# Optimization experiments

Hardware: AMD Instinct MI355X
Metric: run time of the kernel (lower is better)

Reference implementation:

```python
import jax, jax.numpy as jnp
import numpy as np

N_NODES = 100000
N_EDGES = 1600000
IN_CH = 64
HID = 64
N_GRAPHS = 64


def _sage_conv(x, src, dst, Wl, bl, Wr, n_nodes):
    # PyG SAGEConv (aggr='mean'): out = lin_l(mean_{j in N(i)} x_j) + lin_r(x_i)
    msg = x[src]                                            # [E, d] gather
    agg = jax.ops.segment_sum(msg, dst, num_segments=n_nodes)
    cnt = jax.ops.segment_sum(jnp.ones((src.shape[0],), x.dtype), dst,
                              num_segments=n_nodes)
    agg = agg / jnp.maximum(cnt, 1.0)[:, None]
    return agg @ Wl + bl + x @ Wr


def setup_inputs() -> dict:
    key = jax.random.key(0)
    ks = jax.random.split(key, 16)
    x = jax.random.normal(ks[0], (N_NODES, IN_CH), jnp.float32)
    edge_index = jax.random.randint(ks[1], (2, N_EDGES), 0, N_NODES, jnp.int64)
    batch = jnp.sort(jax.random.randint(ks[2], (N_NODES,), 0, N_GRAPHS, jnp.int64))

    def glorot(k, fan_in, fan_out):
        s = jnp.sqrt(2.0 / (fan_in + fan_out))
        return jax.random.normal(k, (fan_in, fan_out), jnp.float32) * s

    params = {
        'W1l': glorot(ks[3], IN_CH, HID), 'b1': jnp.zeros((HID,), jnp.float32),
        'W1r': glorot(ks[4], IN_CH, HID),
        'W2l': glorot(ks[5], HID, HID), 'b2': jnp.zeros((HID,), jnp.float32),
        'W2r': glorot(ks[6], HID, HID),
        'W3l': glorot(ks[7], HID, HID), 'b3': jnp.zeros((HID,), jnp.float32),
        'W3r': glorot(ks[8], HID, HID),
        'Wc1': glorot(ks[9], HID, HID // 2), 'bc1': jnp.zeros((HID // 2,), jnp.float32),
        'Wc2': glorot(ks[10], HID // 2, 2), 'bc2': jnp.zeros((2,), jnp.float32),
    }
    return {'x': x, 'edge_index': edge_index, 'batch': batch, **params}


def reference(x, edge_index, batch,
              W1l, b1, W1r, W2l, b2, W2r, W3l, b3, W3r,
              Wc1, bc1, Wc2, bc2):
    src, dst = edge_index[0], edge_index[1]
    n = x.shape[0]
    h = jax.nn.relu(_sage_conv(x, src, dst, W1l, b1, W1r, n))   # dropout = identity (eval)
    h = jax.nn.relu(_sage_conv(h, src, dst, W2l, b2, W2r, n))
    h = jax.nn.relu(_sage_conv(h, src, dst, W3l, b3, W3r, n))
    # global mean pool over graphs
    sums = jax.ops.segment_sum(h, batch, num_segments=N_GRAPHS)
    cnts = jax.ops.segment_sum(jnp.ones((n,), h.dtype), batch, num_segments=N_GRAPHS)
    g = sums / jnp.maximum(cnts, 1.0)[:, None]                  # [G, HID]
    # MLP head (dropout = identity at eval)
    return jax.nn.relu(g @ Wc1 + bc1) @ Wc2 + bc2               # [G, 2]
```

## Files before the change

kernel.cpp:

```cpp
#include <hip/hip_runtime.h>
#include <hip/hip_bf16.h>
#include <hip/hip_fp16.h>

typedef unsigned int u32;
typedef unsigned short u16;
typedef _Float16 f16x8 __attribute__((ext_vector_type(8)));
typedef float f32x4 __attribute__((ext_vector_type(4)));

#define NBLK1 512
#define CVTBLK 256
#define WPREP 6

__device__ __forceinline__ u16 f2h(float f) { return __half_as_ushort(__float2half(f)); }
__device__ __forceinline__ u32 packh2(float a, float b) {
    return (u32)f2h(a) | ((u32)f2h(b) << 16);
}

__device__ __forceinline__ int gidx(const void* p, long long i, int w64) {
    if (w64) return (int)((const long long*)p)[i];
    return ((const int*)p)[i];
}

__device__ __forceinline__ int detect_w64(const int* edge_words, int E, int tid, int* sh) {
    if (tid == 0) *sh = 0;
    __syncthreads();
    const long long totalWords = 2LL * E;
    const long long step = totalWords / 256;
    long long w = ((long long)tid * step) | 1;
    int nz = (w < totalWords) ? edge_words[w] : 0;
    if (nz) atomicOr(sh, 1);
    __syncthreads();
    return (*sh) ? 0 : 1;
}

__global__ void __launch_bounds__(256) fused_hist_cvt(
        const void* __restrict__ edge, int* __restrict__ flag, u32* __restrict__ ticket,
        u32* __restrict__ HG, int E, int n, int nb1,
        const float* __restrict__ X, u16* __restrict__ Xh,
        const float* __restrict__ W1l, const float* __restrict__ W1r,
        const float* __restrict__ W2l, const float* __restrict__ W2r,
        const float* __restrict__ W3l, const float* __restrict__ W3r,
        _Float16* __restrict__ WFrag) {
    const int tid = threadIdx.x;
    if (blockIdx.x < NBLK1) {
        __shared__ u32 h[256];
        __shared__ int shnz;
        h[tid] = 0;
        const int w64 = detect_w64((const int*)edge, E, tid, &shnz);
        if (blockIdx.x == 0 && tid == 0) { flag[0] = w64; ticket[0] = 0; }
        __syncthreads();
        const int chunk = (E + NBLK1 - 1) / NBLK1;
        const int s = blockIdx.x * chunk;
        const int e = min(s + chunk, E);
        for (int i = s + tid; i < e; i += 256) {
            int d = gidx(edge, (long long)E + i, w64);
            if ((unsigned)d >= (unsigned)n) d = 0;
            atomicAdd(&h[d >> 9], 1);
        }
        __syncthreads();
        for (int b = tid; b < nb1; b += 256) HG[b * NBLK1 + blockIdx.x] = h[b];
        return;
    }
    if (blockIdx.x >= NBLK1 + CVTBLK) {
        const int b = blockIdx.x - NBLK1 - CVTBLK;
        const float* Ws[WPREP] = {W1l, W1r, W2l, W2r, W3l, W3r};
        const float* src = Ws[b];
        _Float16* dst = WFrag + b * 4096;
        for (int idx = tid; idx < 4096; idx += 256) {
            const int k = idx >> 6, c = idx & 63;
            const int d = ((((k >> 5) * 4 + ((k >> 3) & 3)) * 4 + (c >> 4)) * 16 + (c & 15)) * 8
                          + (k & 7);
            dst[d] = (_Float16)src[idx];
        }
        return;
    }
    const long long total4 = (long long)n * 16;
    const long long stride = (long long)CVTBLK * 256;
    long long i = (long long)(blockIdx.x - NBLK1) * 256 + tid;
    const float4* X4 = (const float4*)X;
    uint2* O = (uint2*)Xh;
    for (; i < total4; i += stride) {
        float4 v = X4[i];
        uint2 o;
        o.x = packh2(v.x, v.y);
        o.y = packh2(v.z, v.w);
        O[i] = o;
    }
}

__global__ void scanAB(u32* __restrict__ HG, u32* __restrict__ blockSums,
                       u32* __restrict__ SB, u32* __restrict__ ticket, int n) {
    __shared__ u32 ts[256];
    __shared__ int isLast;
    const int ITEMS = 8;
    const int tid = threadIdx.x;
    int base = blockIdx.x * 2048 + tid * ITEMS;
    u32 v[ITEMS];
    u32 sum = 0;
#pragma unroll
    for (int i = 0; i < ITEMS; ++i) {
        int idx = base + i;
        v[i] = (idx < n) ? HG[idx] : 0;
        sum += v[i];
    }
    ts[tid] = sum;
    __syncthreads();
    u32 incl = sum;
    for (int d = 1; d < 256; d <<= 1) {
        u32 y = 0;
        if (tid >= d) y = ts[tid - d];
        __syncthreads();
        incl += y;
        ts[tid] = incl;
        __syncthreads();
    }
    u32 run = incl - sum;
#pragma unroll
    for (int i = 0; i < ITEMS; ++i) {
        int idx = base + i;
        if (idx < n) HG[idx] = run;
        run += v[i];
    }
    if (tid == 255) {
        atomicExch(&blockSums[blockIdx.x], incl);
        __threadfence();
        u32 t = atomicAdd(&ticket[0], 1u);
        isLast = (t == gridDim.x - 1);
    }
    __syncthreads();
    if (!isLast) return;
    const int nb = gridDim.x;
    u32 bv = (tid < nb) ? atomicAdd(&blockSums[tid], 0u) : 0;
    ts[tid] = bv;
    __syncthreads();
    u32 bincl = bv;
    for (int d = 1; d < 256; d <<= 1) {
        u32 y = 0;
        if (tid >= d) y = ts[tid - d];
        __syncthreads();
        bincl += y;
        ts[tid] = bincl;
        __syncthreads();
    }
    if (tid < nb) SB[tid] = bincl - bv;
}

__global__ void __launch_bounds__(256) p1_scatter(const void* __restrict__ edge,
                                                  const int* __restrict__ flag,
                                                  const u32* __restrict__ HG,
                                                  const u32* __restrict__ SB,
                                                  u32* __restrict__ P, int E, int n, int nb1) {
    __shared__ u32 base[256];
    __shared__ u32 cur[256];
    const int tid = threadIdx.x;
    cur[tid] = 0;
    for (int b = tid; b < nb1; b += 256) {
        int i = b * NBLK1 + blockIdx.x;
        base[b] = HG[i] + SB[i >> 11];
    }
    __syncthreads();
    const int w64 = flag[0];
    const int chunk = (E + NBLK1 - 1) / NBLK1;
    const int s = blockIdx.x * chunk;
    const int e = min(s + chunk, E);
    for (int i = s + tid; i < e; i += 256) {
        int d = gidx(edge, (long long)E + i, w64);
        if ((unsigned)d >= (unsigned)n) d = 0;
        int sv = gidx(edge, i, w64);
        if ((unsigned)sv >= (unsigned)n) sv = 0;
        const int b1 = d >> 9;
        u32 r = atomicAdd(&cur[b1], 1);
        P[base[b1] + r] = (u32)sv | ((u32)(d & 511) << 17);
    }
}

__global__ void __launch_bounds__(512) p2_kernel(const u32* __restrict__ P,
                                                 const u32* __restrict__ HG,
                                                 const u32* __restrict__ SB,
                                                 u32* __restrict__ offs,
                                                 int* __restrict__ ss,
                                                 float* __restrict__ pool,
                                                 int E, int n, int nb1) {
    __shared__ u32 h2[512];
    __shared__ u32 ts[512];
    const int tid = threadIdx.x;
    const int b = blockIdx.x;
    if (b == 0)
        for (int i = tid; i < 4096; i += 512) pool[i] = 0.f;
    const int i0 = b * NBLK1;
    const int bs = (int)(HG[i0] + SB[i0 >> 11]);
    int be;
    if (b + 1 < nb1) {
        const int i1 = (b + 1) * NBLK1;
        be = (int)(HG[i1] + SB[i1 >> 11]);
    } else be = E;
    h2[tid] = 0;
    __syncthreads();
    for (int i = bs + tid; i < be; i += 512) atomicAdd(&h2[(P[i] >> 17) & 511], 1);
    __syncthreads();
    u32 v = h2[tid];
    ts[tid] = v;
    __syncthreads();
    u32 incl = v;
    for (int d = 1; d < 512; d <<= 1) {
        u32 y = 0;
        if (tid >= d) y = ts[tid - d];
        __syncthreads();
        incl += y;
        ts[tid] = incl;
        __syncthreads();
    }
    u32 run = incl - v;
    h2[tid] = run;
    const int node0 = b * 512 + tid;
    if (node0 < n) offs[node0] = bs + run;
    if (b == 0 && tid == 0) offs[n] = (u32)E;
    __syncthreads();
    for (int i = bs + tid; i < be; i += 512) {
        u32 p = P[i];
        u32 r = atomicAdd(&h2[(p >> 17) & 511], 1);
        ss[bs + r] = (int)(p & 0x1FFFFu);
    }
}

__global__ void __launch_bounds__(256) sage4(
        const u16* __restrict__ G, const u32* __restrict__ offs,
        const int* __restrict__ ss,
        const _Float16* __restrict__ WF,
        const float* __restrict__ Bv,
        u16* __restrict__ Hout, float* __restrict__ pool,
        const void* __restrict__ batch, const int* __restrict__ flag,
        int n, int mode) {
    __shared__ _Float16 XL[2][16][72];
    const int tid = threadIdx.x;
    const int wv = tid >> 6;
    const int tIdx = wv >> 1;
    const int half = wv & 1;
    const int lane = tid & 63;
    const int quad = lane >> 4;
    const int m16 = lane & 15;
    const int cb = half * 32 + quad * 8;
    const int w64 = mode ? flag[0] : 0;

    const int ntiles = (n + 15) >> 4;
    const int npairs = (ntiles + 1) >> 1;
    for (int pair = blockIdx.x; pair < npairs; pair += gridDim.x) {
        const int tile = pair * 2 + tIdx;
        const int tvalid = tile < ntiles;
        const int nodeBase = tile << 4;
        const int node_m = nodeBase + m16;
        const int valid = tvalid && node_m < n;
        const int nodeA = valid ? node_m : n - 1;
        const u32 o0 = offs[nodeA];
        const int deg = valid ? (int)(offs[nodeA + 1] - o0) : 0;
        const int* sp = ss + o0;
        f16x8 s;
#pragma unroll
        for (int j = 0; j < 8; ++j) s[j] = (_Float16)0;
        int e = 0;
        for (; e + 4 <= deg; e += 4) {
            const int iA = sp[e], iB = sp[e + 1], iC = sp[e + 2], iD = sp[e + 3];
            f16x8 a = *(const f16x8*)(G + ((size_t)iA << 6) + cb);
            f16x8 b = *(const f16x8*)(G + ((size_t)iB << 6) + cb);
            f16x8 c = *(const f16x8*)(G + ((size_t)iC << 6) + cb);
            f16x8 d = *(const f16x8*)(G + ((size_t)iD << 6) + cb);
            s += a; s += b; s += c; s += d;
        }
        for (; e < deg; ++e)
            s += *(const f16x8*)(G + ((size_t)(sp[e]) << 6) + cb);
        const float rdf = deg > 0 ? 1.f / (float)deg : 0.f;
        const _Float16 hrd = (_Float16)rdf;
#pragma unroll
        for (int j = 0; j < 8; ++j) s[j] *= hrd;
        *(f16x8*)(&XL[tIdx][m16][cb]) = s;
        __syncthreads();
        int zz;
        asm volatile("v_mov_b32 %0, 0" : "=v"(zz));
        const f16x8 soth = *(const f16x8*)(&XL[tIdx][m16][(half ^ 1) * 32 + quad * 8]);
        const f16x8 s0 = half ? soth : s;
        const f16x8 s1 = half ? s : soth;
        if (tvalid) {
            const _Float16* wlp = WF + zz + quad * 512 + m16 * 8;
            const _Float16* wrp = wlp + 4096;
            const u16* gs = G + ((size_t)nodeA << 6) + zz;
            const f16x8 as0 = *(const f16x8*)(gs + quad * 8);
            const f16x8 as1 = *(const f16x8*)(gs + 32 + quad * 8);
#pragma unroll 1
            for (int tt = 0; tt < 2; ++tt) {
                const int t = half * 2 + tt;
                const f16x8 l0 = *(const f16x8*)(wlp + t * 128);
                const f16x8 l1 = *(const f16x8*)(wlp + 2048 + t * 128);
                const f16x8 r0 = *(const f16x8*)(wrp + t * 128);
                const f16x8 r1 = *(const f16x8*)(wrp + 2048 + t * 128);
                const float bt = Bv[t * 16 + m16];
                f32x4 acc = {bt, bt, bt, bt};
                acc = __builtin_amdgcn_mfma_f32_16x16x32_f16(s0, l0, acc, 0, 0, 0);
                acc = __builtin_amdgcn_mfma_f32_16x16x32_f16(s1, l1, acc, 0, 0, 0);
                acc = __builtin_amdgcn_mfma_f32_16x16x32_f16(as0, r0, acc, 0, 0, 0);
                acc = __builtin_amdgcn_mfma_f32_16x16x32_f16(as1, r1, acc, 0, 0, 0);
                if (mode == 0) {
#pragma unroll
                    for (int rg = 0; rg < 4; ++rg) {
                        const int node = nodeBase + quad * 4 + rg;
                        if (node < n)
                            Hout[(size_t)node * 64 + t * 16 + m16] = f2h(fmaxf(acc[rg], 0.f));
                    }
                } else {
                    float v0 = fmaxf(acc[0], 0.f), v1 = fmaxf(acc[1], 0.f);
                    float v2 = fmaxf(acc[2], 0.f), v3 = fmaxf(acc[3], 0.f);
                    const int lastN = nodeBase + 15 < n ? nodeBase + 15 : n - 1;
                    const int g0 = gidx(batch, nodeBase, w64) & 63;
                    const int g1 = gidx(batch, lastN, w64) & 63;
                    if (nodeBase + 15 < n && g0 == g1) {
                        float cs = v0 + v1 + v2 + v3;
                        cs += __shfl_xor(cs, 16, 64);
                        cs += __shfl_xor(cs, 32, 64);
                        if (quad == 0) atomicAdd(&pool[g0 * 64 + t * 16 + m16], cs);
                    } else {
                        const float vv[4] = {v0, v1, v2, v3};
#pragma unroll
                        for (int rg = 0; rg < 4; ++rg) {
                            const int node = nodeBase + quad * 4 + rg;
                            if (node < n) {
                                const int g = gidx(batch, node, w64) & 63;
                                atomicAdd(&pool[g * 64 + t * 16 + m16], vv[rg]);
                            }
                        }
                    }
                }
            }
        }
        __syncthreads();
    }
}

__global__ void head_kernel(const float* __restrict__ pool, const void* __restrict__ batch,
                            const int* __restrict__ flag,
                            const float* __restrict__ Wc1, const float* __restrict__ bc1,
                            const float* __restrict__ Wc2, const float* __restrict__ bc2,
                            float* __restrict__ out, int n) {
    __shared__ float gm[64 * 64];
    __shared__ float am[64 * 32];
    __shared__ int cnts[64];
    const int tid = threadIdx.x;
    const int w64 = flag[0];
    if (tid < 64) {
        int lo = 0, hi = n;
        while (lo < hi) { int mid = (lo + hi) >> 1; if (gidx(batch, mid, w64) < tid) lo = mid + 1; else hi = mid; }
        int lo2 = 0, hi2 = n;
        int v2 = tid + 1;
        while (lo2 < hi2) { int mid = (lo2 + hi2) >> 1; if (gidx(batch, mid, w64) < v2) lo2 = mid + 1; else hi2 = mid; }
        cnts[tid] = lo2 - lo;
    }
    __syncthreads();
    for (int i = tid; i < 4096; i += 256) {
        int g = i >> 6;
        float c = (float)(cnts[g] > 0 ? cnts[g] : 1);
        gm[i] = pool[i] / c;
    }
    __syncthreads();
    for (int i = tid; i < 64 * 32; i += 256) {
        int g = i >> 5, j = i & 31;
        float acc = bc1[j];
        for (int k = 0; k < 64; ++k) acc += gm[g * 64 + k] * Wc1[k * 32 + j];
        am[i] = acc > 0.f ? acc : 0.f;
    }
    __syncthreads();
    if (tid < 128) {
        int g = tid >> 1, o = tid & 1;
        float acc = bc2[o];
        for (int j = 0; j < 32; ++j) acc += am[g * 32 + j] * Wc2[j * 2 + o];
        out[tid] = acc;
    }
}

extern "C" void kernel_launch(void* const* d_in, const int* in_sizes, int n_in,
                              void* d_out, int out_size, void* d_ws, size_t ws_size,
                              hipStream_t stream) {
    const float* x   = (const float*)d_in[0];
    const void* edge = d_in[1];
    const void* batch = d_in[2];
    const float* W1l = (const float*)d_in[3];
    const float* b1  = (const float*)d_in[4];
    const float* W1r = (const float*)d_in[5];
    const float* W2l = (const float*)d_in[6];
    const float* b2  = (const float*)d_in[7];
    const float* W2r = (const float*)d_in[8];
    const float* W3l = (const float*)d_in[9];
    const float* b3  = (const float*)d_in[10];
    const float* W3r = (const float*)d_in[11];
    const float* Wc1 = (const float*)d_in[12];
    const float* bc1 = (const float*)d_in[13];
    const float* Wc2 = (const float*)d_in[14];
    const float* bc2 = (const float*)d_in[15];

    const int n = in_sizes[0] / 64;
    const int E = in_sizes[1] / 2;
    const int nb1 = (n + 511) >> 9;
    const int NS = nb1 * NBLK1;

    char* w = (char*)d_ws;
    size_t o = 0;
    auto take = [&](size_t bytes) -> void* {
        void* p = w + o;
        o = (o + bytes + 511) & ~(size_t)511;
        return p;
    };
    int* flag      = (int*)take(sizeof(int));
    u32* ticket    = (u32*)take(2 * sizeof(u32));
    u32* offs      = (u32*)take((size_t)(n + 1) * sizeof(u32));
    u32* HG        = (u32*)take((size_t)(NS + 1) * sizeof(u32));
    u32* blockSums = (u32*)take(256 * sizeof(u32));
    u32* SB        = (u32*)take(256 * sizeof(u32));
    u32* P         = (u32*)take((size_t)E * sizeof(u32));
    int* ss        = (int*)take((size_t)E * sizeof(int));
    u16* Xh        = (u16*)take((size_t)n * 64 * sizeof(u16));
    u16* HA        = (u16*)take((size_t)n * 64 * sizeof(u16));
    u16* HB        = (u16*)take((size_t)n * 64 * sizeof(u16));
    _Float16* WF   = (_Float16*)take(WPREP * 4096 * sizeof(_Float16));
    float* pool    = (float*)take(64 * 64 * sizeof(float));

    fused_hist_cvt<<<NBLK1 + CVTBLK + WPREP, 256, 0, stream>>>(
        edge, flag, ticket, HG, E, n, nb1, x, Xh, W1l, W1r, W2l, W2r, W3l, W3r, WF);
    const int nbScan = (NS + 2047) / 2048;
    scanAB<<<nbScan, 256, 0, stream>>>(HG, blockSums, SB, ticket, NS);
    p1_scatter<<<NBLK1, 256, 0, stream>>>(edge, flag, HG, SB, P, E, n, nb1);
    p2_kernel<<<nb1, 512, 0, stream>>>(P, HG, SB, offs, ss, pool, E, n, nb1);

    const int ntiles = (n + 15) >> 4;
    const int npairs = (ntiles + 1) >> 1;
    sage4<<<npairs, 256, 0, stream>>>(Xh, offs, ss, WF, b1, HA, nullptr,
                                      batch, flag, n, 0);
    sage4<<<npairs, 256, 0, stream>>>(HA, offs, ss, WF + 2 * 4096, b2, HB, nullptr,
                                      batch, flag, n, 0);
    sage4<<<npairs, 256, 0, stream>>>(HB, offs, ss, WF + 4 * 4096, b3, nullptr, pool,
                                      batch, flag, n, 1);
    head_kernel<<<1, 256, 0, stream>>>(pool, batch, flag, Wc1, bc1, Wc2, bc2,
                                       (float*)d_out, n);
}
```

Measured before the change: 302.8 us.

## Stage CSR scatter writes in shared memory for coalesced global stores

p1_scatter now does a local histogram and prefix scan of its edge chunk. It bucket-sorts packed edges into an LDS buffer, then copies each bucket to its global slot contiguously, one wavefront per bucket. p2_kernel likewise sorts source indices into a 12288-entry LDS buffer and writes them out linearly, spilling to direct stores on overflow. The goal is to replace scattered, uncoalesced global writes with contiguous ones. The cost is a second read of the dst indices and much more LDS use, which can lower occupancy. p1 has no overflow guard if an edge chunk exceeds its buffer size.

```diff
diff --git a/kernel.cpp b/kernel.cpp
--- a/kernel.cpp
+++ b/kernel.cpp
@@ -10,6 +10,8 @@
 #define NBLK1 512
 #define CVTBLK 256
 #define WPREP 6
+#define P1BUF 3456
+#define P2BUF 12288
 
 __device__ __forceinline__ u16 f2h(float f) { return __half_as_ushort(__float2half(f)); }
 __device__ __forceinline__ u32 packh2(float a, float b) {
@@ -150,14 +152,12 @@
                                                   const u32* __restrict__ HG,
                                                   const u32* __restrict__ SB,
                                                   u32* __restrict__ P, int E, int n, int nb1) {
-    __shared__ u32 base[256];
-    __shared__ u32 cur[256];
-    const int tid = threadIdx.x;
-    cur[tid] = 0;
-    for (int b = tid; b < nb1; b += 256) {
-        int i = b * NBLK1 + blockIdx.x;
-        base[b] = HG[i] + SB[i >> 11];
-    }
+    __shared__ u32 lcnt[256];
+    __shared__ u32 lstart[256];
+    __shared__ u32 lpos[256];
+    __shared__ u32 buf[P1BUF];
+    const int tid = threadIdx.x;
+    lcnt[tid] = 0;
     __syncthreads();
     const int w64 = flag[0];
     const int chunk = (E + NBLK1 - 1) / NBLK1;
@@ -166,11 +166,43 @@
     for (int i = s + tid; i < e; i += 256) {
         int d = gidx(edge, (long long)E + i, w64);
         if ((unsigned)d >= (unsigned)n) d = 0;
+        atomicAdd(&lcnt[d >> 9], 1);
+    }
+    __syncthreads();
+    u32 v = lcnt[tid];
+    buf[tid] = v;
+    __syncthreads();
+    u32 incl = v;
+    for (int d = 1; d < 256; d <<= 1) {
+        u32 y = 0;
+        if (tid >= d) y = buf[tid - d];
+        __syncthreads();
+        incl += y;
+        buf[tid] = incl;
+        __syncthreads();
+    }
+    lstart[tid] = incl - v;
+    lpos[tid] = incl - v;
+    __syncthreads();
+    for (int i = s + tid; i < e; i += 256) {
+        int d = gidx(edge, (long long)E + i, w64);
+        if ((unsigned)d >= (unsigned)n) d = 0;
         int sv = gidx(edge, i, w64);
         if ((unsigned)sv >= (unsigned)n) sv = 0;
         const int b1 = d >> 9;
-        u32 r = atomicAdd(&cur[b1], 1);
-        P[base[b1] + r] = (u32)sv | ((u32)(d & 511) << 17);
+        u32 r = atomicAdd(&lpos[b1], 1);
+        buf[r] = (u32)sv | ((u32)(d & 511) << 17);
+    }
+    __syncthreads();
+    const int wv = tid >> 6;
+    const int lane = tid & 63;
+    for (int b = wv; b < nb1; b += 4) {
+        const u32 cnt = lcnt[b];
+        if (cnt == 0) continue;
+        const int gi = b * NBLK1 + blockIdx.x;
+        const u32 gbase = HG[gi] + SB[gi >> 11];
+        const u32 lbase = lstart[b];
+        for (u32 i = lane; i < cnt; i += 64) P[gbase + i] = buf[lbase + i];
     }
 }
 
@@ -183,6 +215,7 @@
                                                  int E, int n, int nb1) {
     __shared__ u32 h2[512];
     __shared__ u32 ts[512];
+    __shared__ u32 sbuf[P2BUF];
     const int tid = threadIdx.x;
     const int b = blockIdx.x;
     if (b == 0)
@@ -219,8 +252,14 @@
     for (int i = bs + tid; i < be; i += 512) {
         u32 p = P[i];
         u32 r = atomicAdd(&h2[(p >> 17) & 511], 1);
-        ss[bs + r] = (int)(p & 0x1FFFFu);
-    }
+        u32 srcv = p & 0x1FFFFu;
+        if (r < P2BUF) sbuf[r] = srcv;
+        else ss[bs + r] = (int)srcv;
+    }
+    __syncthreads();
+    const int bsize = be - bs;
+    const int m = bsize < P2BUF ? bsize : P2BUF;
+    for (int i = tid; i < m; i += 512) ss[bs + i] = (int)sbuf[i];
 }
 
 __global__ void __launch_bounds__(256) sage4(
```

New measurement: 318.9 us. 1.05x slower.

## Replace two-pass bucketed CSR build with global atomic count-scan-place

Applied to the files above, without the earlier changes.

Replaces the two-level bucket histogram, scatter and per-bucket local sort with a direct per-node degree count using global atomics, a scan over node counts, and a placement pass using per-node atomic ranks. This drops the intermediate P buffer and one full pass over the edges, at the cost of heavy global atomic contention and random writes. Neighbour ordering within a node becomes nondeterministic. It also switches the neighbour-sum accumulation in the SAGE layers from fp16 to fp32, which costs extra convert instructions but improves accuracy.

```diff
diff --git a/kernel.cpp b/kernel.cpp
--- a/kernel.cpp
+++ b/kernel.cpp
@@ -7,9 +7,11 @@
 typedef _Float16 f16x8 __attribute__((ext_vector_type(8)));
 typedef float f32x4 __attribute__((ext_vector_type(4)));
 
-#define NBLK1 512
+#define ZBLK 64
 #define CVTBLK 256
 #define WPREP 6
+#define CNTBLK 512
+#define PLCBLK 512
 
 __device__ __forceinline__ u16 f2h(float f) { return __half_as_ushort(__float2half(f)); }
 __device__ __forceinline__ u32 packh2(float a, float b) {
@@ -33,36 +35,29 @@
     return (*sh) ? 0 : 1;
 }
 
-__global__ void __launch_bounds__(256) fused_hist_cvt(
+__global__ void __launch_bounds__(256) k1_zero_cvt(
         const void* __restrict__ edge, int* __restrict__ flag, u32* __restrict__ ticket,
-        u32* __restrict__ HG, int E, int n, int nb1,
+        u32* __restrict__ C, int E, int n,
         const float* __restrict__ X, u16* __restrict__ Xh,
         const float* __restrict__ W1l, const float* __restrict__ W1r,
         const float* __restrict__ W2l, const float* __restrict__ W2r,
         const float* __restrict__ W3l, const float* __restrict__ W3r,
         _Float16* __restrict__ WFrag) {
     const int tid = threadIdx.x;
-    if (blockIdx.x < NBLK1) {
-        __shared__ u32 h[256];
-        __shared__ int shnz;
-        h[tid] = 0;
-        const int w64 = detect_w64((const int*)edge, E, tid, &shnz);
-        if (blockIdx.x == 0 && tid == 0) { flag[0] = w64; ticket[0] = 0; }
-        __syncthreads();
-        const int chunk = (E + NBLK1 - 1) / NBLK1;
-        const int s = blockIdx.x * chunk;
-        const int e = min(s + chunk, E);
-        for (int i = s + tid; i < e; i += 256) {
-            int d = gidx(edge, (long long)E + i, w64);
-            if ((unsigned)d >= (unsigned)n) d = 0;
-            atomicAdd(&h[d >> 9], 1);
-        }
-        __syncthreads();
-        for (int b = tid; b < nb1; b += 256) HG[b * NBLK1 + blockIdx.x] = h[b];
+    if (blockIdx.x < ZBLK) {
+        if (blockIdx.x == 0) {
+            __shared__ int shnz;
+            const int w64 = detect_w64((const int*)edge, E, tid, &shnz);
+            if (tid == 0) { flag[0] = w64; ticket[0] = 0; }
+        }
+        const int nq = (n + 3) >> 2;
+        const uint4 z4 = {0, 0, 0, 0};
+        for (int i = blockIdx.x * 256 + tid; i < nq; i += ZBLK * 256)
+            ((uint4*)C)[i] = z4;
         return;
     }
-    if (blockIdx.x >= NBLK1 + CVTBLK) {
-        const int b = blockIdx.x - NBLK1 - CVTBLK;
+    if (blockIdx.x >= ZBLK + CVTBLK) {
+        const int b = blockIdx.x - ZBLK - CVTBLK;
         const float* Ws[WPREP] = {W1l, W1r, W2l, W2r, W3l, W3r};
         const float* src = Ws[b];
         _Float16* dst = WFrag + b * 4096;
@@ -76,7 +71,7 @@
     }
     const long long total4 = (long long)n * 16;
     const long long stride = (long long)CVTBLK * 256;
-    long long i = (long long)(blockIdx.x - NBLK1) * 256 + tid;
+    long long i = (long long)(blockIdx.x - ZBLK) * 256 + tid;
     const float4* X4 = (const float4*)X;
     uint2* O = (uint2*)Xh;
     for (; i < total4; i += stride) {
@@ -85,6 +80,24 @@
         o.x = packh2(v.x, v.y);
         o.y = packh2(v.z, v.w);
         O[i] = o;
+    }
+}
+
+__global__ void __launch_bounds__(256) count_kernel(
+        const void* __restrict__ edge, const int* __restrict__ flag,
+        u32* __restrict__ C, u32* __restrict__ rank, float* __restrict__ pool,
+        int E, int n) {
+    const int w64 = flag[0];
+    const int gid = blockIdx.x * 256 + threadIdx.x;
+    const int tot = gridDim.x * 256;
+    const int nq = (n + 3) >> 2;
+    const uint4 z4 = {0, 0, 0, 0};
+    for (int i = gid; i < nq; i += tot) ((uint4*)rank)[i] = z4;
+    if (gid < 4096) pool[gid] = 0.f;
+    for (int i = gid; i < E; i += tot) {
+        int d = gidx(edge, (long long)E + i, w64);
+        if ((unsigned)d >= (unsigned)n) d = 0;
+        atomicAdd(&C[d], 1u);
     }
 }
 
@@ -145,81 +158,23 @@
     if (tid < nb) SB[tid] = bincl - bv;
 }
 
-__global__ void __launch_bounds__(256) p1_scatter(const void* __restrict__ edge,
-                                                  const int* __restrict__ flag,
-                                                  const u32* __restrict__ HG,
-                                                  const u32* __restrict__ SB,
-                                                  u32* __restrict__ P, int E, int n, int nb1) {
-    __shared__ u32 base[256];
-    __shared__ u32 cur[256];
-    const int tid = threadIdx.x;
-    cur[tid] = 0;
-    for (int b = tid; b < nb1; b += 256) {
-        int i = b * NBLK1 + blockIdx.x;
-        base[b] = HG[i] + SB[i >> 11];
-    }
-    __syncthreads();
+__global__ void __launch_bounds__(256) place_kernel(
+        const void* __restrict__ edge, const int* __restrict__ flag,
+        const u32* __restrict__ C, const u32* __restrict__ SB,
+        u32* __restrict__ rank, u32* __restrict__ offs, int* __restrict__ ss,
+        int E, int n) {
     const int w64 = flag[0];
-    const int chunk = (E + NBLK1 - 1) / NBLK1;
-    const int s = blockIdx.x * chunk;
-    const int e = min(s + chunk, E);
-    for (int i = s + tid; i < e; i += 256) {
+    const int gid = blockIdx.x * 256 + threadIdx.x;
+    const int tot = gridDim.x * 256;
+    for (int i = gid; i < n; i += tot) offs[i] = C[i] + SB[i >> 11];
+    if (gid == 0) offs[n] = (u32)E;
+    for (int i = gid; i < E; i += tot) {
         int d = gidx(edge, (long long)E + i, w64);
         if ((unsigned)d >= (unsigned)n) d = 0;
         int sv = gidx(edge, i, w64);
         if ((unsigned)sv >= (unsigned)n) sv = 0;
-        const int b1 = d >> 9;
-        u32 r = atomicAdd(&cur[b1], 1);
-        P[base[b1] + r] = (u32)sv | ((u32)(d & 511) << 17);
-    }
-}
-
-__global__ void __launch_bounds__(512) p2_kernel(const u32* __restrict__ P,
-                                                 const u32* __restrict__ HG,
-                                                 const u32* __restrict__ SB,
-                                                 u32* __restrict__ offs,
-                                                 int* __restrict__ ss,
-                                                 float* __restrict__ pool,
-                                                 int E, int n, int nb1) {
-    __shared__ u32 h2[512];
-    __shared__ u32 ts[512];
-    const int tid = threadIdx.x;
-    const int b = blockIdx.x;
-    if (b == 0)
-        for (int i = tid; i < 4096; i += 512) pool[i] = 0.f;
-    const int i0 = b * NBLK1;
-    const int bs = (int)(HG[i0] + SB[i0 >> 11]);
-    int be;
-    if (b + 1 < nb1) {
-        const int i1 = (b + 1) * NBLK1;
-        be = (int)(HG[i1] + SB[i1 >> 11]);
-    } else be = E;
-    h2[tid] = 0;
-    __syncthreads();
-    for (int i = bs + tid; i < be; i += 512) atomicAdd(&h2[(P[i] >> 17) & 511], 1);
-    __syncthreads();
-    u32 v = h2[tid];
-    ts[tid] = v;
-    __syncthreads();
-    u32 incl = v;
-    for (int d = 1; d < 512; d <<= 1) {
-        u32 y = 0;
-        if (tid >= d) y = ts[tid - d];
-        __syncthreads();
-        incl += y;
-        ts[tid] = incl;
-        __syncthreads();
-    }
-    u32 run = incl - v;
-    h2[tid] = run;
-    const int node0 = b * 512 + tid;
-    if (node0 < n) offs[node0] = bs + run;
-    if (b == 0 && tid == 0) offs[n] = (u32)E;
-    __syncthreads();
-    for (int i = bs + tid; i < be; i += 512) {
-        u32 p = P[i];
-        u32 r = atomicAdd(&h2[(p >> 17) & 511], 1);
-        ss[bs + r] = (int)(p & 0x1FFFFu);
+        const u32 p = C[d] + SB[d >> 11] + atomicAdd(&rank[d], 1u);
+        ss[p] = sv;
     }
 }
 
@@ -254,9 +209,9 @@
         const u32 o0 = offs[nodeA];
         const int deg = valid ? (int)(offs[nodeA + 1] - o0) : 0;
         const int* sp = ss + o0;
-        f16x8 s;
-#pragma unroll
-        for (int j = 0; j < 8; ++j) s[j] = (_Float16)0;
+        float sa[8];
+#pragma unroll
+        for (int j = 0; j < 8; ++j) sa[j] = 0.f;
         int e = 0;
         for (; e + 4 <= deg; e += 4) {
             const int iA = sp[e], iB = sp[e + 1], iC = sp[e + 2], iD = sp[e + 3];
@@ -264,14 +219,19 @@
             f16x8 b = *(const f16x8*)(G + ((size_t)iB << 6) + cb);
             f16x8 c = *(const f16x8*)(G + ((size_t)iC << 6) + cb);
             f16x8 d = *(const f16x8*)(G + ((size_t)iD << 6) + cb);
-            s += a; s += b; s += c; s += d;
-        }
-        for (; e < deg; ++e)
-            s += *(const f16x8*)(G + ((size_t)(sp[e]) << 6) + cb);
+#pragma unroll
+            for (int j = 0; j < 8; ++j)
+                sa[j] += (float)a[j] + (float)b[j] + ((float)c[j] + (float)d[j]);
+        }
+        for (; e < deg; ++e) {
+            f16x8 a = *(const f16x8*)(G + ((size_t)(sp[e]) << 6) + cb);
+#pragma unroll
+            for (int j = 0; j < 8; ++j) sa[j] += (float)a[j];
+        }
         const float rdf = deg > 0 ? 1.f / (float)deg : 0.f;
-        const _Float16 hrd = (_Float16)rdf;
-#pragma unroll
-        for (int j = 0; j < 8; ++j) s[j] *= hrd;
+        f16x8 s;
+#pragma unroll
+        for (int j = 0; j < 8; ++j) s[j] = (_Float16)(sa[j] * rdf);
         *(f16x8*)(&XL[tIdx][m16][cb]) = s;
         __syncthreads();
         int zz;
@@ -396,8 +356,6 @@
 
     const int n = in_sizes[0] / 64;
     const int E = in_sizes[1] / 2;
-    const int nb1 = (n + 511) >> 9;
-    const int NS = nb1 * NBLK1;
 
     char* w = (char*)d_ws;
     size_t o = 0;
@@ -408,11 +366,11 @@
     };
     int* flag      = (int*)take(sizeof(int));
     u32* ticket    = (u32*)take(2 * sizeof(u32));
+    u32* C         = (u32*)take(((size_t)n + 4) * sizeof(u32));
+    u32* rank      = (u32*)take(((size_t)n + 4) * sizeof(u32));
     u32* offs      = (u32*)take((size_t)(n + 1) * sizeof(u32));
-    u32* HG        = (u32*)take((size_t)(NS + 1) * sizeof(u32));
     u32* blockSums = (u32*)take(256 * sizeof(u32));
     u32* SB        = (u32*)take(256 * sizeof(u32));
-    u32* P         = (u32*)take((size_t)E * sizeof(u32));
     int* ss        = (int*)take((size_t)E * sizeof(int));
     u16* Xh        = (u16*)take((size_t)n * 64 * sizeof(u16));
     u16* HA        = (u16*)take((size_t)n * 64 * sizeof(u16));
@@ -420,12 +378,12 @@
     _Float16* WF   = (_Float16*)take(WPREP * 4096 * sizeof(_Float16));
     float* pool    = (float*)take(64 * 64 * sizeof(float));
 
-    fused_hist_cvt<<<NBLK1 + CVTBLK + WPREP, 256, 0, stream>>>(
-        edge, flag, ticket, HG, E, n, nb1, x, Xh, W1l, W1r, W2l, W2r, W3l, W3r, WF);
-    const int nbScan = (NS + 2047) / 2048;
-    scanAB<<<nbScan, 256, 0, stream>>>(HG, blockSums, SB, ticket, NS);
-    p1_scatter<<<NBLK1, 256, 0, stream>>>(edge, flag, HG, SB, P, E, n, nb1);
-    p2_kernel<<<nb1, 512, 0, stream>>>(P, HG, SB, offs, ss, pool, E, n, nb1);
+    k1_zero_cvt<<<ZBLK + CVTBLK + WPREP, 256, 0, stream>>>(
+        edge, flag, ticket, C, E, n, x, Xh, W1l, W1r, W2l, W2r, W3l, W3r, WF);
+    count_kernel<<<CNTBLK, 256, 0, stream>>>(edge, flag, C, rank, pool, E, n);
+    const int nbScan = (n + 2047) / 2048;
+    scanAB<<<nbScan, 256, 0, stream>>>(C, blockSums, SB, ticket, n);
+    place_kernel<<<PLCBLK, 256, 0, stream>>>(edge, flag, C, SB, rank, offs, ss, E, n);
 
     const int ntiles = (n + 15) >> 4;
     const int npairs = (ntiles + 1) >> 1;
```

After: 414.8 us. 1.37x slower.
